# Kernel optimization log

Hardware: AMD Instinct MI355X
Metric: run time of the kernel (lower is better)

## Reference

```python
import jax, jax.numpy as jnp
import numpy as np

EMBEDDING_DIM = 256
CODEBOOK_SIZE = 1024
COMMITMENT_COST = 0.25


def setup_inputs() -> dict:
    key = jax.random.key(0)
    k1, k2 = jax.random.split(key)
    inputs = jax.random.normal(k1, (16, 4096, EMBEDDING_DIM), dtype=jnp.float32)
    embeddings = jax.random.normal(k2, (EMBEDDING_DIM, CODEBOOK_SIZE), dtype=jnp.float32)
    return {"inputs": inputs, "embeddings": embeddings}


def reference(inputs, embeddings):
    # inputs: [B, T, D]; embeddings: [D, K]
    D = embeddings.shape[0]
    K = embeddings.shape[1]
    flat = inputs.reshape(-1, D)  # [N, D]

    sim = flat @ embeddings
    dists = (jnp.sum(flat * flat, axis=1, keepdims=True)
             + jnp.sum(embeddings * embeddings, axis=0)
             - 2.0 * sim)
    flat_idx = jnp.argmin(dists, axis=1)  # [N]

    encodings = jax.nn.one_hot(flat_idx, K, dtype=jnp.float32)  # [N, K]
    encoding_indices = flat_idx.reshape(inputs.shape[:-1])  # [B, T]

    # embedding lookup: gather rows of embeddings^T -> [B, T, D]
    quantized = jnp.take(embeddings.T, encoding_indices, axis=0)

    e_latent_loss = jnp.mean(jnp.square(jax.lax.stop_gradient(quantized) - inputs))
    q_latent_loss = jnp.mean(jnp.square(quantized - jax.lax.stop_gradient(inputs)))
    loss = q_latent_loss + COMMITMENT_COST * e_latent_loss

    # straight-through estimator
    quantized_st = inputs + jax.lax.stop_gradient(quantized - inputs)

    return quantized_st, encodings, encoding_indices, loss
```

## Files before the change

### kernel.cpp

```cpp
#include <hip/hip_runtime.h>

#define N_ROWS 65536
#define DIM    256
#define KCB    1024

#define Q_OFF    0
#define ENC_OFF  (N_ROWS * DIM)
#define IDX_OFF  (ENC_OFF + N_ROWS * KCB)
#define LOSS_OFF (IDX_OFF + N_ROWS)

#define ET_OFF   (ENC_OFF + 0)
#define NRM_OFF  (ENC_OFF + 262144)
#define IDXI_OFF (ENC_OFF + 263168)
#define PART_OFF (ENC_OFF + 328704)
#define AMB_OFF  (ENC_OFF + 345088)
#define PMIN_OFF (ENC_OFF + 524288)
#define A2_OFF   (ENC_OFF + 4718592)
#define BST_OFF  (ENC_OFF + 21495808)

#define TAU 0.05f

typedef short  bf16x8 __attribute__((ext_vector_type(8)));
typedef float  f32x4  __attribute__((ext_vector_type(4)));
typedef unsigned short u16x8 __attribute__((ext_vector_type(8)));
#define AS1 __attribute__((address_space(1)))
#define AS3 __attribute__((address_space(3)))

__device__ inline unsigned short f2bf(float x) {
    unsigned u = __float_as_uint(x);
    return (unsigned short)((u + 0x7FFFu + ((u >> 16) & 1u)) >> 16);
}
__device__ inline float bf2f(unsigned short b) {
    return __uint_as_float(((unsigned)b) << 16);
}

__global__ __launch_bounds__(256)
void vq_prep_a(const float* __restrict__ X, float* __restrict__ out) {
    unsigned short* A2 = (unsigned short*)(out + A2_OFF);
    int gid = blockIdx.x * 256 + threadIdx.x;
    int row = gid >> 5;
    int d0  = (gid & 31) * 8;
    const float* xp = X + (size_t)row * DIM + d0;
    float4 v0 = *(const float4*)xp;
    float4 v1 = *(const float4*)(xp + 4);
    float xv[8] = {v0.x, v0.y, v0.z, v0.w, v1.x, v1.y, v1.z, v1.w};
    u16x8 h, l;
#pragma unroll
    for (int i = 0; i < 8; ++i) {
        unsigned short hb = f2bf(xv[i]);
        h[i] = hb;
        l[i] = f2bf(xv[i] - bf2f(hb));
    }
    *(u16x8*)(A2 + (size_t)row * 512 + d0) = h;
    *(u16x8*)(A2 + (size_t)row * 512 + 256 + d0) = l;
}

__global__ __launch_bounds__(64)
void vq_prep_b(const float* __restrict__ E, float* __restrict__ out) {
    float* ET  = out + ET_OFF;
    float* nrm = out + NRM_OFF;
    unsigned short* B2 = (unsigned short*)(out + BST_OFF);
    const int k = blockIdx.x, t = threadIdx.x;
    float v[4]; float s = 0.f;
    ushort4 hb, lb;
#pragma unroll
    for (int i = 0; i < 4; ++i) {
        float e = E[(size_t)(t * 4 + i) * KCB + k];
        v[i] = e; s += e * e;
        unsigned short h = f2bf(e);
        ((unsigned short*)&hb)[i] = h;
        ((unsigned short*)&lb)[i] = f2bf(e - bf2f(h));
    }
    *(float4*)(ET + (size_t)k * DIM + t * 4) = *(float4*)v;
    *(ushort4*)(B2 + (size_t)k * 512 + t * 4) = hb;
    *(ushort4*)(B2 + (size_t)k * 512 + 256 + t * 4) = lb;
#pragma unroll
    for (int off = 32; off >= 1; off >>= 1) s += __shfl_xor(s, off);
    if (t == 0) nrm[k] = s;
    if (k == 0 && t == 0) ((int*)(out + AMB_OFF))[0] = 0;
}

__global__ __launch_bounds__(256, 3)
void vq_gemm(float* __restrict__ out) {
    __shared__ short lds[16384];
    const unsigned short* A2 = (const unsigned short*)(out + A2_OFF);
    const unsigned short* B2 = (const unsigned short*)(out + BST_OFF);
    const float* nrm = out + NRM_OFF;
    float4* pmin = (float4*)(out + PMIN_OFF);

    const int orig = blockIdx.x;
    const int mapped = (orig & 7) * 512 + (orig >> 3);
    const int rb = mapped >> 3, cb = mapped & 7;
    const int row0 = rb * 128, col0 = cb * 128;

    const int tid = threadIdx.x;
    const int lane = tid & 63, l15 = lane & 15, lhi = lane >> 4;
    const int w = tid >> 6, wr = w >> 1, wc = w & 1;

    f32x4 acc[4][4];
#pragma unroll
    for (int i = 0; i < 4; ++i)
#pragma unroll
        for (int j = 0; j < 4; ++j) acc[i][j] = (f32x4){0.f, 0.f, 0.f, 0.f};

    const int sr = tid >> 3;
    const int sk = (tid & 7) * 8;
    const int wofs = (tid & 192) * 16;

    for (int ks = 0; ks < 12; ++ks) {
        const int phase = ks >> 2, kr = (ks & 3) * 64;
        const int ak = (phase == 2 ? 256 : 0) + kr;
        const int bk = (phase == 1 ? 256 : 0) + kr;
        __syncthreads();
#pragma unroll
        for (int i = 0; i < 4; ++i) {
            int r = i * 32 + sr;
            __builtin_amdgcn_global_load_lds(
                (const AS1 unsigned*)(A2 + (size_t)(row0 + r) * 512 + ak + sk),
                (AS3 unsigned*)((char*)lds + i * 4096 + wofs), 16, 0, 0);
        }
#pragma unroll
        for (int i = 0; i < 4; ++i) {
            int r = i * 32 + sr;
            __builtin_amdgcn_global_load_lds(
                (const AS1 unsigned*)(B2 + (size_t)(col0 + r) * 512 + bk + sk),
                (AS3 unsigned*)((char*)lds + 16384 + i * 4096 + wofs), 16, 0, 0);
        }
        asm volatile("s_waitcnt vmcnt(0)" ::: "memory");
        __syncthreads();
#pragma unroll
        for (int kk = 0; kk < 2; ++kk) {
            bf16x8 af[4], bfr[4];
#pragma unroll
            for (int mi = 0; mi < 4; ++mi)
                af[mi] = *(const bf16x8*)&lds[(wr * 64 + mi * 16 + l15) * 64 + kk * 32 + lhi * 8];
#pragma unroll
            for (int ni = 0; ni < 4; ++ni)
                bfr[ni] = *(const bf16x8*)&lds[8192 + (wc * 64 + ni * 16 + l15) * 64 + kk * 32 + lhi * 8];
#pragma unroll
            for (int mi = 0; mi < 4; ++mi)
#pragma unroll
                for (int ni = 0; ni < 4; ++ni)
                    acc[mi][ni] = __builtin_amdgcn_mfma_f32_16x16x32_bf16(
                        af[mi], bfr[ni], acc[mi][ni], 0, 0, 0);
        }
    }

    float nv[4];
#pragma unroll
    for (int ni = 0; ni < 4; ++ni) nv[ni] = nrm[col0 + wc * 64 + ni * 16 + l15];
#pragma unroll
    for (int mi = 0; mi < 4; ++mi)
#pragma unroll
        for (int j = 0; j < 4; ++j) {
            float a = 3.4e38f, b = 3.4e38f; int ia = 0;
#pragma unroll
            for (int ni = 0; ni < 4; ++ni) {
                float dist = fmaf(-2.f, acc[mi][ni][j], nv[ni]);
                int col = col0 + wc * 64 + ni * 16 + l15;
                if (dist < a) { b = a; a = dist; ia = col; }
                else if (dist < b) b = dist;
            }
#pragma unroll
            for (int off = 1; off < 16; off <<= 1) {
                float oa = __shfl_xor(a, off);
                float ob = __shfl_xor(b, off);
                int   oi = __shfl_xor(ia, off);
                if (oa < a || (oa == a && oi < ia)) { b = fminf(a, ob); a = oa; ia = oi; }
                else b = fminf(b, oa);
            }
            if (l15 == 0) {
                int grow = row0 + wr * 64 + mi * 16 + lhi * 4 + j;
                float4 pv;
                pv.x = a; pv.y = b; pv.z = __int_as_float(ia); pv.w = 0.f;
                pmin[(size_t)grow * 16 + cb * 2 + wc] = pv;
            }
        }
}

__global__ __launch_bounds__(256)
void vq_combine(float* __restrict__ out) {
    const float4* pmin = (const float4*)(out + PMIN_OFF);
    int* idxi = (int*)(out + IDXI_OFF);
    int* amb  = (int*)(out + AMB_OFF);
    const int row = blockIdx.x * 256 + threadIdx.x;
    float a = 3.4e38f, b = 3.4e38f; int ia = 0;
#pragma unroll
    for (int s = 0; s < 16; ++s) {
        float4 p = pmin[(size_t)row * 16 + s];
        int oi = __float_as_int(p.z);
        if (p.x < a || (p.x == a && oi < ia)) { b = fminf(a, p.y); a = p.x; ia = oi; }
        else b = fminf(b, p.x);
    }
    idxi[row] = ia;
    if (b - a < TAU) {
        int pos = atomicAdd(amb, 1);
        if (pos < 65536) amb[1 + pos] = row;
    }
}

__global__ __launch_bounds__(256)
void vq_rescore(const float* __restrict__ X, const float* __restrict__ E,
                float* __restrict__ out) {
    __shared__ float xs[256];
    __shared__ float rv[256];
    __shared__ int   ri[256];
    const float* nrm = out + NRM_OFF;
    const int* amb = (const int*)(out + AMB_OFF);
    int* idxi = (int*)(out + IDXI_OFF);
    int count = amb[0]; if (count > 65536) count = 65536;
    for (int it = blockIdx.x; it < count; it += gridDim.x) {
        const int row = amb[1 + it];
        __syncthreads();
        xs[threadIdx.x] = X[(size_t)row * DIM + threadIdx.x];
        __syncthreads();
        float best = 3.4e38f; int bi = 0;
        for (int cc = 0; cc < 4; ++cc) {
            const int code = cc * 256 + threadIdx.x;
            float acc = 0.f;
            for (int d = 0; d < 256; ++d)
                acc = fmaf(xs[d], E[(size_t)d * KCB + code], acc);
            float dist = fmaf(-2.f, acc, nrm[code]);
            if (dist < best) { best = dist; bi = code; }
        }
        rv[threadIdx.x] = best; ri[threadIdx.x] = bi;
        __syncthreads();
        for (int off = 128; off > 0; off >>= 1) {
            if (threadIdx.x < off) {
                float ov = rv[threadIdx.x + off]; int oi = ri[threadIdx.x + off];
                if (ov < rv[threadIdx.x] || (ov == rv[threadIdx.x] && oi < ri[threadIdx.x])) {
                    rv[threadIdx.x] = ov; ri[threadIdx.x] = oi;
                }
            }
            __syncthreads();
        }
        if (threadIdx.x == 0) idxi[row] = ri[0];
    }
}

__global__ __launch_bounds__(256)
void vq_outputs(const float* __restrict__ X, float* __restrict__ out) {
    const float* ET  = out + ET_OFF;
    const int*   idx = (const int*)(out + IDXI_OFF);
    float*       part = out + PART_OFF;
    __shared__ float red[4];
    const int row  = blockIdx.x * 4 + (threadIdx.x >> 6);
    const int lane = threadIdx.x & 63;
    const int id   = idx[row];
    float4 e = *(const float4*)(ET + (size_t)id * DIM + lane * 4);
    float4 x = *(const float4*)(X + (size_t)row * DIM + lane * 4);
    float dx = e.x - x.x, dy = e.y - x.y, dz = e.z - x.z, dw = e.w - x.w;
    float4 q;
    q.x = x.x + dx; q.y = x.y + dy; q.z = x.z + dz; q.w = x.w + dw;
    *(float4*)(out + Q_OFF + (size_t)row * DIM + lane * 4) = q;
    float s = dx * dx + dy * dy + dz * dz + dw * dw;
#pragma unroll
    for (int off = 32; off >= 1; off >>= 1) s += __shfl_xor(s, off);
    if (lane == 0) {
        red[threadIdx.x >> 6] = s;
        out[IDX_OFF + row] = (float)id;
    }
    __syncthreads();
    if (threadIdx.x == 0) part[blockIdx.x] = red[0] + red[1] + red[2] + red[3];
}

__global__ __launch_bounds__(256)
void vq_loss(float* __restrict__ out) {
    const float* part = out + PART_OFF;
    __shared__ double red[256];
    const int tid = threadIdx.x;
    double s = 0.0;
    for (int i = tid; i < 16384; i += 256) s += (double)part[i];
    red[tid] = s;
    __syncthreads();
    for (int off = 128; off > 0; off >>= 1) {
        if (tid < off) red[tid] += red[tid + off];
        __syncthreads();
    }
    if (tid == 0)
        out[LOSS_OFF] = (float)(1.25 * red[0] / (double)((size_t)N_ROWS * DIM));
}

__global__ __launch_bounds__(256)
void vq_encodings(float* __restrict__ out) {
    const float* idxf = out + IDX_OFF;
    float4* enc4 = (float4*)(out + ENC_OFF);
    const size_t total4 = (size_t)N_ROWS * KCB / 4;
    const size_t stride = (size_t)gridDim.x * blockDim.x;
    for (size_t g = (size_t)blockIdx.x * blockDim.x + threadIdx.x; g < total4; g += stride) {
        int n  = (int)(g >> 8);
        int c0 = ((int)g & 255) * 4;
        int r  = (int)idxf[n] - c0;
        float4 v;
        v.x = (r == 0) ? 1.f : 0.f;
        v.y = (r == 1) ? 1.f : 0.f;
        v.z = (r == 2) ? 1.f : 0.f;
        v.w = (r == 3) ? 1.f : 0.f;
        enc4[g] = v;
    }
}

extern "C" void kernel_launch(void* const* d_in, const int* in_sizes, int n_in,
                              void* d_out, int out_size, void* d_ws, size_t ws_size,
                              hipStream_t stream) {
    const float* X = (const float*)d_in[0];
    const float* E = (const float*)d_in[1];
    float* out = (float*)d_out;

    vq_prep_a   <<<8192, 256, 0, stream>>>(X, out);
    vq_prep_b   <<<1024,  64, 0, stream>>>(E, out);
    vq_gemm     <<<4096, 256, 0, stream>>>(out);
    vq_combine  <<<256,  256, 0, stream>>>(out);
    vq_rescore  <<<2048, 256, 0, stream>>>(X, E, out);
    vq_outputs  <<<16384, 256, 0, stream>>>(X, out);
    vq_loss     <<<1,    256, 0, stream>>>(out);
    vq_encodings<<<2048, 256, 0, stream>>>(out);
}
```

Baseline: 644.8 us.

## Swizzle LDS, share A tile across split-bf16 B passes, warp-level rescore

```diff
diff --git a/kernel.cpp b/kernel.cpp
--- a/kernel.cpp
+++ b/kernel.cpp
@@ -82,7 +82,7 @@
 
 __global__ __launch_bounds__(256, 3)
 void vq_gemm(float* __restrict__ out) {
-    __shared__ short lds[16384];
+    __shared__ short lds[24576];
     const unsigned short* A2 = (const unsigned short*)(out + A2_OFF);
     const unsigned short* B2 = (const unsigned short*)(out + BST_OFF);
     const float* nrm = out + NRM_OFF;
@@ -96,6 +96,7 @@
     const int tid = threadIdx.x;
     const int lane = tid & 63, l15 = lane & 15, lhi = lane >> 4;
     const int w = tid >> 6, wr = w >> 1, wc = w & 1;
+    const int swz = (l15 & 7) * 8;
 
     f32x4 acc[4][4];
 #pragma unroll
@@ -103,48 +104,77 @@
 #pragma unroll
         for (int j = 0; j < 4; ++j) acc[i][j] = (f32x4){0.f, 0.f, 0.f, 0.f};
 
-    const int sr = tid >> 3;
-    const int sk = (tid & 7) * 8;
+    const int sr   = tid >> 3;
+    const int sksw = ((tid & 7) ^ ((tid >> 3) & 7)) * 8;
     const int wofs = (tid & 192) * 16;
 
-    for (int ks = 0; ks < 12; ++ks) {
-        const int phase = ks >> 2, kr = (ks & 3) * 64;
-        const int ak = (phase == 2 ? 256 : 0) + kr;
-        const int bk = (phase == 1 ? 256 : 0) + kr;
-        __syncthreads();
-#pragma unroll
-        for (int i = 0; i < 4; ++i) {
-            int r = i * 32 + sr;
-            __builtin_amdgcn_global_load_lds(
-                (const AS1 unsigned*)(A2 + (size_t)(row0 + r) * 512 + ak + sk),
-                (AS3 unsigned*)((char*)lds + i * 4096 + wofs), 16, 0, 0);
-        }
-#pragma unroll
-        for (int i = 0; i < 4; ++i) {
-            int r = i * 32 + sr;
-            __builtin_amdgcn_global_load_lds(
-                (const AS1 unsigned*)(B2 + (size_t)(col0 + r) * 512 + bk + sk),
-                (AS3 unsigned*)((char*)lds + 16384 + i * 4096 + wofs), 16, 0, 0);
-        }
+#define STAGE4(SRC, R0, KOFF, LDSB)                                           \
+    _Pragma("unroll")                                                         \
+    for (int i = 0; i < 4; ++i) {                                             \
+        __builtin_amdgcn_global_load_lds(                                     \
+            (const AS1 unsigned*)((SRC) + (size_t)((R0) + i * 32 + sr) * 512  \
+                                  + (KOFF) + sksw),                           \
+            (AS3 unsigned*)((char*)lds + (LDSB) + i * 4096 + wofs), 16, 0, 0);\
+    }
+
+    for (int kr = 0; kr < 4; ++kr) {
+        __syncthreads();
+        STAGE4(A2, row0, kr * 64, 0);
+        STAGE4(B2, col0, kr * 64, 16384);
+        STAGE4(B2, col0, 256 + kr * 64, 32768);
         asm volatile("s_waitcnt vmcnt(0)" ::: "memory");
         __syncthreads();
 #pragma unroll
         for (int kk = 0; kk < 2; ++kk) {
-            bf16x8 af[4], bfr[4];
-#pragma unroll
-            for (int mi = 0; mi < 4; ++mi)
-                af[mi] = *(const bf16x8*)&lds[(wr * 64 + mi * 16 + l15) * 64 + kk * 32 + lhi * 8];
-#pragma unroll
-            for (int ni = 0; ni < 4; ++ni)
-                bfr[ni] = *(const bf16x8*)&lds[8192 + (wc * 64 + ni * 16 + l15) * 64 + kk * 32 + lhi * 8];
+            const int cofs = (kk * 32 + lhi * 8) ^ swz;
+            bf16x8 af[4], bh[4], bl[4];
+#pragma unroll
+            for (int mi = 0; mi < 4; ++mi)
+                af[mi] = *(const bf16x8*)&lds[(wr * 64 + mi * 16 + l15) * 64 + cofs];
+#pragma unroll
+            for (int ni = 0; ni < 4; ++ni) {
+                bh[ni] = *(const bf16x8*)&lds[8192 + (wc * 64 + ni * 16 + l15) * 64 + cofs];
+                bl[ni] = *(const bf16x8*)&lds[16384 + (wc * 64 + ni * 16 + l15) * 64 + cofs];
+            }
 #pragma unroll
             for (int mi = 0; mi < 4; ++mi)
 #pragma unroll
                 for (int ni = 0; ni < 4; ++ni)
                     acc[mi][ni] = __builtin_amdgcn_mfma_f32_16x16x32_bf16(
-                        af[mi], bfr[ni], acc[mi][ni], 0, 0, 0);
-        }
-    }
+                        af[mi], bh[ni], acc[mi][ni], 0, 0, 0);
+#pragma unroll
+            for (int mi = 0; mi < 4; ++mi)
+#pragma unroll
+                for (int ni = 0; ni < 4; ++ni)
+                    acc[mi][ni] = __builtin_amdgcn_mfma_f32_16x16x32_bf16(
+                        af[mi], bl[ni], acc[mi][ni], 0, 0, 0);
+        }
+    }
+    for (int kr = 0; kr < 4; ++kr) {
+        __syncthreads();
+        STAGE4(A2, row0, 256 + kr * 64, 0);
+        STAGE4(B2, col0, kr * 64, 16384);
+        asm volatile("s_waitcnt vmcnt(0)" ::: "memory");
+        __syncthreads();
+#pragma unroll
+        for (int kk = 0; kk < 2; ++kk) {
+            const int cofs = (kk * 32 + lhi * 8) ^ swz;
+            bf16x8 af[4], bh[4];
+#pragma unroll
+            for (int mi = 0; mi < 4; ++mi)
+                af[mi] = *(const bf16x8*)&lds[(wr * 64 + mi * 16 + l15) * 64 + cofs];
+#pragma unroll
+            for (int ni = 0; ni < 4; ++ni)
+                bh[ni] = *(const bf16x8*)&lds[8192 + (wc * 64 + ni * 16 + l15) * 64 + cofs];
+#pragma unroll
+            for (int mi = 0; mi < 4; ++mi)
+#pragma unroll
+                for (int ni = 0; ni < 4; ++ni)
+                    acc[mi][ni] = __builtin_amdgcn_mfma_f32_16x16x32_bf16(
+                        af[mi], bh[ni], acc[mi][ni], 0, 0, 0);
+        }
+    }
+#undef STAGE4
 
     float nv[4];
 #pragma unroll
@@ -200,41 +230,40 @@
 }
 
 __global__ __launch_bounds__(256)
-void vq_rescore(const float* __restrict__ X, const float* __restrict__ E,
-                float* __restrict__ out) {
-    __shared__ float xs[256];
-    __shared__ float rv[256];
-    __shared__ int   ri[256];
+void vq_rescore(const float* __restrict__ X, float* __restrict__ out) {
+    __shared__ float xs[4][256];
+    const float* ET  = out + ET_OFF;
     const float* nrm = out + NRM_OFF;
     const int* amb = (const int*)(out + AMB_OFF);
     int* idxi = (int*)(out + IDXI_OFF);
+    const int wid = threadIdx.x >> 6, lane = threadIdx.x & 63;
     int count = amb[0]; if (count > 65536) count = 65536;
-    for (int it = blockIdx.x; it < count; it += gridDim.x) {
+    for (int it = blockIdx.x * 4 + wid; it < count; it += gridDim.x * 4) {
         const int row = amb[1 + it];
-        __syncthreads();
-        xs[threadIdx.x] = X[(size_t)row * DIM + threadIdx.x];
-        __syncthreads();
+        *(float4*)&xs[wid][lane * 4] = *(const float4*)(X + (size_t)row * DIM + lane * 4);
         float best = 3.4e38f; int bi = 0;
-        for (int cc = 0; cc < 4; ++cc) {
-            const int code = cc * 256 + threadIdx.x;
+        for (int cc = 0; cc < 16; ++cc) {
+            const int code = cc * 64 + lane;
+            const float* ep = ET + (size_t)code * DIM;
             float acc = 0.f;
-            for (int d = 0; d < 256; ++d)
-                acc = fmaf(xs[d], E[(size_t)d * KCB + code], acc);
+#pragma unroll
+            for (int d = 0; d < 256; d += 4) {
+                float4 ev = *(const float4*)(ep + d);
+                acc = fmaf(xs[wid][d],     ev.x, acc);
+                acc = fmaf(xs[wid][d + 1], ev.y, acc);
+                acc = fmaf(xs[wid][d + 2], ev.z, acc);
+                acc = fmaf(xs[wid][d + 3], ev.w, acc);
+            }
             float dist = fmaf(-2.f, acc, nrm[code]);
             if (dist < best) { best = dist; bi = code; }
         }
-        rv[threadIdx.x] = best; ri[threadIdx.x] = bi;
-        __syncthreads();
-        for (int off = 128; off > 0; off >>= 1) {
-            if (threadIdx.x < off) {
-                float ov = rv[threadIdx.x + off]; int oi = ri[threadIdx.x + off];
-                if (ov < rv[threadIdx.x] || (ov == rv[threadIdx.x] && oi < ri[threadIdx.x])) {
-                    rv[threadIdx.x] = ov; ri[threadIdx.x] = oi;
-                }
-            }
-            __syncthreads();
-        }
-        if (threadIdx.x == 0) idxi[row] = ri[0];
+#pragma unroll
+        for (int off = 1; off < 64; off <<= 1) {
+            float ov = __shfl_xor(best, off);
+            int   oi = __shfl_xor(bi, off);
+            if (ov < best || (ov == best && oi < bi)) { best = ov; bi = oi; }
+        }
+        if (lane == 0) idxi[row] = bi;
     }
 }
 
@@ -311,7 +340,7 @@
     vq_prep_b   <<<1024,  64, 0, stream>>>(E, out);
     vq_gemm     <<<4096, 256, 0, stream>>>(out);
     vq_combine  <<<256,  256, 0, stream>>>(out);
-    vq_rescore  <<<2048, 256, 0, stream>>>(X, E, out);
+    vq_rescore  <<<1024, 256, 0, stream>>>(X, out);
     vq_outputs  <<<16384, 256, 0, stream>>>(X, out);
     vq_loss     <<<1,    256, 0, stream>>>(out);
     vq_encodings<<<2048, 256, 0, stream>>>(out);
```

After: 709.1 us. +10.0%, slower.
